# Kernel optimization log

Measured on AMD Instinct MI355X. Metric: run time of the kernel, lower is better.

## Reference

```python
import jax, jax.numpy as jnp
import numpy as np

B, T, ENC, DEC, ATTN = 64, 2048, 512, 512, 256


def setup_inputs() -> dict:
    key = jax.random.key(0)
    k1, k2, k3, k4, k5, k6 = jax.random.split(key, 6)
    enc_out = jax.random.normal(k1, (B, T, ENC), dtype=jnp.float32)
    dec_hidden = jax.random.normal(k2, (B, DEC), dtype=jnp.float32)
    mask = jax.random.randint(k3, (B, T), 0, 2) == 1  # True = masked out
    # learned params (Linear with bias=False); torch Linear weight is [out,in],
    # we store transposed [in,out] for x @ W convention
    s_enc = 1.0 / np.sqrt(ENC)
    s_dec = 1.0 / np.sqrt(DEC)
    s_v = 1.0 / np.sqrt(ATTN)
    W_enc = jax.random.uniform(k4, (ENC, ATTN), jnp.float32, -s_enc, s_enc)
    W_dec = jax.random.uniform(k5, (DEC, ATTN), jnp.float32, -s_dec, s_dec)
    v = jax.random.uniform(k6, (ATTN,), jnp.float32, -s_v, s_v)
    return {"enc_out": enc_out, "dec_hidden": dec_hidden, "mask": mask,
            "W_enc": W_enc, "W_dec": W_dec, "v": v}


def reference(enc_out, dec_hidden, mask, W_enc, W_dec, v):
    # proj_enc: [B,T,A]; proj_dec: [B,1,A]
    proj_enc = jnp.einsum('bte,ea->bta', enc_out, W_enc)
    proj_dec = jnp.einsum('bd,da->ba', dec_hidden, W_dec)[:, None, :]
    # energy: [B,T] -- additive (Bahdanau) score
    energy = jnp.einsum('bta,a->bt', jnp.tanh(proj_enc + proj_dec), v)
    energy = jnp.where(mask, -jnp.inf, energy)
    attn_w = jax.nn.softmax(energy, axis=-1)
    attn_w = jnp.nan_to_num(attn_w, nan=0.0)  # fully-masked rows -> 0
    context = jnp.einsum('bt,bte->be', attn_w, enc_out)
    return context, attn_w
```

## Files before the change

### kernel.cpp

```cpp
#include <hip/hip_runtime.h>
#include <stdint.h>

#define Bx 64
#define Tx 2048
#define ENCx 512
#define ATTx 256

typedef float f4 __attribute__((ext_vector_type(4)));
typedef float f32x4 __attribute__((ext_vector_type(4)));
typedef short bf16x8 __attribute__((ext_vector_type(8)));
typedef __fp16 h2 __attribute__((ext_vector_type(2)));

__device__ __forceinline__ unsigned short f2bf(float f) {
  union { float f; uint32_t u; } c; c.f = f;
  uint32_t u = c.u;
  u += 0x7fffu + ((u >> 16) & 1u);
  return (unsigned short)(u >> 16);
}

__device__ __forceinline__ uint32_t pk_bf(float lo, float hi) {
  uint32_t a = __float_as_uint(lo) + 0x8000u;
  uint32_t b = __float_as_uint(hi) + 0x8000u;
  return __builtin_amdgcn_perm(b, a, 0x07060302u);
}

__device__ __forceinline__ uint32_t pk_f16(float lo, float hi) {
  h2 r = __builtin_amdgcn_cvt_pkrtz(lo, hi);
  union { h2 h; uint32_t u; } c; c.h = r;
  return c.u;
}

__device__ __forceinline__ float ftanh(float x) {
  x = fminf(8.f, fmaxf(-8.f, x));
  float z = __expf(2.f * x);
  return 1.f - __fdividef(2.f, z + 1.f);
}

__global__ void k0_wt(const float* __restrict__ W, unsigned short* __restrict__ WTc) {
  int tid = blockIdx.x * 256 + threadIdx.x;
  int kc = tid >> 13;
  int r = tid & 8191;
  int n = r >> 5;
  int kk = r & 31;
  WTc[tid] = f2bf(W[(kc * 32 + kk) * ATTx + n]);
}

__global__ void k1_pd(const float* __restrict__ dec, const float* __restrict__ Wd,
                      float* __restrict__ pd) {
  __shared__ float ld[512];
  int b = blockIdx.x, a = threadIdx.x;
  ld[a] = dec[b * 512 + a];
  ld[a + 256] = dec[b * 512 + a + 256];
  __syncthreads();
  float s = 0.f;
#pragma unroll 8
  for (int d = 0; d < 512; ++d) s = fmaf(ld[d], Wd[d * ATTx + a], s);
  pd[b * ATTx + a] = s;
}

__global__ __launch_bounds__(128, 1) void k2_fused(
    const float* __restrict__ enc, const unsigned short* __restrict__ WTc,
    const float* __restrict__ pd, const float* __restrict__ v,
    const int* __restrict__ mask, float* __restrict__ energy,
    float* __restrict__ part, float* __restrict__ mloc, float* __restrict__ lloc) {
  __shared__ float pdv[256];
  __shared__ float vvs[256];
  __shared__ unsigned short enc_s[64 * 512];
  __shared__ float e_lds[64];
  __shared__ float wl[64];

  const int tid = threadIdx.x;
  const int wid = tid >> 6;
  const int lane = tid & 63;
  const int q = lane >> 4;
  const int c15 = lane & 15;
  const int m0 = blockIdx.x * 64;
  const int b = m0 >> 11;
  const int chunk = blockIdx.x & 31;

  pdv[tid] = pd[b * ATTx + tid];
  pdv[tid + 128] = pd[b * ATTx + tid + 128];
  vvs[tid] = v[tid];
  vvs[tid + 128] = v[tid + 128];
  __syncthreads();

  const int r0 = wid * 32 + c15;
  const int mrow = m0 + r0;
  const float* a0p = enc + (size_t)mrow * ENCx + q * 8;
  const float* a1p = a0p + 16 * ENCx;
  const unsigned short* wb = WTc + c15 * 32 + q * 8;

  uint4* enc16 = (uint4*)enc_s;
  const int sw = r0 & 7;
  const int w0base = r0 * 64 + q;
  const int w1base = (r0 + 16) * 64 + q;

  f32x4 acc[2][16];
#pragma unroll
  for (int mt = 0; mt < 2; ++mt)
#pragma unroll
    for (int ct = 0; ct < 16; ++ct) { f32x4 z = {0.f,0.f,0.f,0.f}; acc[mt][ct] = z; }

  f4 x0 = *(const f4*)(a0p);
  f4 x1 = *(const f4*)(a0p + 4);
  f4 y0 = *(const f4*)(a1p);
  f4 y1 = *(const f4*)(a1p + 4);

  for (int kc = 0; kc < 16; ++kc) {
    bf16x8 bfr[16];
    const unsigned short* wkc = wb + kc * 8192;
#pragma unroll
    for (int ct = 0; ct < 16; ++ct)
      bfr[ct] = *(const bf16x8*)(wkc + ct * 512);

    const int kn = (kc < 15) ? kc + 1 : 15;
    f4 nx0 = *(const f4*)(a0p + kn * 32);
    f4 nx1 = *(const f4*)(a0p + kn * 32 + 4);
    f4 ny0 = *(const f4*)(a1p + kn * 32);
    f4 ny1 = *(const f4*)(a1p + kn * 32 + 4);

    uint4 hp0, hp1;
    hp0.x = pk_f16(x0.x, x0.y); hp0.y = pk_f16(x0.z, x0.w);
    hp0.z = pk_f16(x1.x, x1.y); hp0.w = pk_f16(x1.z, x1.w);
    hp1.x = pk_f16(y0.x, y0.y); hp1.y = pk_f16(y0.z, y0.w);
    hp1.z = pk_f16(y1.x, y1.y); hp1.w = pk_f16(y1.z, y1.w);
    enc16[(w0base + kc * 4) ^ sw] = hp0;
    enc16[(w1base + kc * 4) ^ sw] = hp1;

    union { uint32_t u[4]; bf16x8 v; } am0, am1;
    am0.u[0] = pk_bf(x0.x, x0.y); am0.u[1] = pk_bf(x0.z, x0.w);
    am0.u[2] = pk_bf(x1.x, x1.y); am0.u[3] = pk_bf(x1.z, x1.w);
    am1.u[0] = pk_bf(y0.x, y0.y); am1.u[1] = pk_bf(y0.z, y0.w);
    am1.u[2] = pk_bf(y1.x, y1.y); am1.u[3] = pk_bf(y1.z, y1.w);

#pragma unroll
    for (int ct = 0; ct < 16; ++ct) {
      acc[0][ct] = __builtin_amdgcn_mfma_f32_16x16x32_bf16(am0.v, bfr[ct], acc[0][ct], 0, 0, 0);
      acc[1][ct] = __builtin_amdgcn_mfma_f32_16x16x32_bf16(am1.v, bfr[ct], acc[1][ct], 0, 0, 0);
    }
    x0 = nx0; x1 = nx1; y0 = ny0; y1 = ny1;
  }

  float ps[2][4];
#pragma unroll
  for (int mt = 0; mt < 2; ++mt)
#pragma unroll
    for (int i = 0; i < 4; ++i) ps[mt][i] = 0.f;
#pragma unroll
  for (int ct = 0; ct < 16; ++ct) {
    float pv = pdv[ct * 16 + c15];
    float vv = vvs[ct * 16 + c15];
#pragma unroll
    for (int mt = 0; mt < 2; ++mt)
#pragma unroll
      for (int i = 0; i < 4; ++i)
        ps[mt][i] += ftanh(acc[mt][ct][i] + pv) * vv;
  }
#pragma unroll
  for (int s = 1; s < 16; s <<= 1)
#pragma unroll
    for (int mt = 0; mt < 2; ++mt)
#pragma unroll
      for (int i = 0; i < 4; ++i)
        ps[mt][i] += __shfl_xor(ps[mt][i], s, 64);
  if (c15 == 0) {
#pragma unroll
    for (int mt = 0; mt < 2; ++mt)
#pragma unroll
      for (int i = 0; i < 4; ++i) {
        int lr = wid * 32 + mt * 16 + q * 4 + i;
        int gm = m0 + lr;
        float ev = mask[gm] ? -1e30f : ps[mt][i];
        energy[gm] = ev;
        e_lds[lr] = ev;
      }
  }
  __syncthreads();

  float ev = e_lds[lane];
  float mx = ev;
#pragma unroll
  for (int s = 1; s < 64; s <<= 1) mx = fmaxf(mx, __shfl_xor(mx, s, 64));
  float w = (ev < -1e29f) ? 0.f : __expf(ev - mx);
  float ls = w;
#pragma unroll
  for (int s = 1; s < 64; s <<= 1) ls += __shfl_xor(ls, s, 64);
  if (wid == 0) wl[lane] = w;
  if (tid == 0) { mloc[b * 32 + chunk] = mx; lloc[b * 32 + chunk] = ls; }
  __syncthreads();

  const uint32_t* encu = (const uint32_t*)enc_s;
  float a0 = 0.f, a1 = 0.f, a2 = 0.f, a3 = 0.f;
#pragma unroll 4
  for (int t = 0; t < 64; ++t) {
    float wv = wl[t];
    int xr = (t & 7) << 2;
    uint32_t p0 = encu[(t * 256 + tid) ^ xr];
    uint32_t p1 = encu[(t * 256 + tid + 128) ^ xr];
    union { uint32_t u; h2 h; } c0, c1;
    c0.u = p0; c1.u = p1;
    a0 = fmaf((float)c0.h.x, wv, a0);
    a1 = fmaf((float)c0.h.y, wv, a1);
    a2 = fmaf((float)c1.h.x, wv, a2);
    a3 = fmaf((float)c1.h.y, wv, a3);
  }
  float* pp = part + (size_t)(chunk * 64 + b) * 512;
  float2 s0; s0.x = a0; s0.y = a1;
  float2 s1; s1.x = a2; s1.y = a3;
  *(float2*)(pp + 2 * tid) = s0;
  *(float2*)(pp + 2 * tid + 256) = s1;
}

__global__ void k3_merge(const float* __restrict__ energy, const float* __restrict__ part,
                         const float* __restrict__ mloc, const float* __restrict__ lloc,
                         float* __restrict__ attn, float* __restrict__ ctx) {
  __shared__ float redm[4];
  __shared__ float redl[4];
  __shared__ float sc[32];
  int b = blockIdx.x, tid = threadIdx.x;
  int lane = tid & 63, wid = tid >> 6;

  float e[8];
#pragma unroll
  for (int i = 0; i < 8; ++i) e[i] = energy[b * Tx + tid + i * 256];
  float m = e[0];
#pragma unroll
  for (int i = 1; i < 8; ++i) m = fmaxf(m, e[i]);
#pragma unroll
  for (int s = 1; s < 64; s <<= 1) m = fmaxf(m, __shfl_xor(m, s, 64));
  if (lane == 0) redm[wid] = m;
  __syncthreads();
  m = fmaxf(fmaxf(redm[0], redm[1]), fmaxf(redm[2], redm[3]));
  bool dead = (m < -1e29f);
  float w[8];
  float l = 0.f;
#pragma unroll
  for (int i = 0; i < 8; ++i) { w[i] = dead ? 0.f : __expf(e[i] - m); l += w[i]; }
#pragma unroll
  for (int s = 1; s < 64; s <<= 1) l += __shfl_xor(l, s, 64);
  if (lane == 0) redl[wid] = l;
  __syncthreads();
  l = redl[0] + redl[1] + redl[2] + redl[3];
  float inv = dead ? 0.f : __fdividef(1.f, l);
#pragma unroll
  for (int i = 0; i < 8; ++i) attn[b * Tx + tid + i * 256] = w[i] * inv;

  if (tid < 64) {
    float mc = (lane < 32) ? mloc[b * 32 + lane] : -3e38f;
    float lc = (lane < 32) ? lloc[b * 32 + lane] : 0.f;
    float mg = mc;
#pragma unroll
    for (int s = 1; s < 64; s <<= 1) mg = fmaxf(mg, __shfl_xor(mg, s, 64));
    float sl = (lane < 32) ? lc * __expf(mc - mg) : 0.f;
    float lg = sl;
#pragma unroll
    for (int s = 1; s < 64; s <<= 1) lg += __shfl_xor(lg, s, 64);
    float ig = (lg > 0.f) ? __fdividef(1.f, lg) : 0.f;
    if (lane < 32) sc[lane] = __expf(mc - mg) * ig;
  }
  __syncthreads();
  float2 a; a.x = 0.f; a.y = 0.f;
  const float* pb = part + (size_t)b * 512 + tid * 2;
#pragma unroll 8
  for (int c = 0; c < 32; ++c) {
    float2 p = *(const float2*)(pb + (size_t)c * 64 * 512);
    float s = sc[c];
    a.x = fmaf(p.x, s, a.x);
    a.y = fmaf(p.y, s, a.y);
  }
  *(float2*)(ctx + b * 512 + tid * 2) = a;
}

extern "C" void kernel_launch(void* const* d_in, const int* in_sizes, int n_in,
                              void* d_out, int out_size, void* d_ws, size_t ws_size,
                              hipStream_t stream) {
  const float* enc   = (const float*)d_in[0];
  const float* dec   = (const float*)d_in[1];
  const int*   mask  = (const int*)d_in[2];
  const float* W_enc = (const float*)d_in[3];
  const float* W_dec = (const float*)d_in[4];
  const float* v     = (const float*)d_in[5];
  float* ctx  = (float*)d_out;
  float* attn = ctx + Bx * ENCx;
  char* ws = (char*)d_ws;
  unsigned short* WTc = (unsigned short*)ws;
  float* pd     = (float*)(ws + 262144);
  float* energy = (float*)(ws + 262144 + 65536);
  float* part   = (float*)(ws + 851968);
  float* mloc   = (float*)(ws + 851968 + 4194304);
  float* lloc   = (float*)(ws + 851968 + 4194304 + 8192);

  k0_wt<<<512, 256, 0, stream>>>(W_enc, WTc);
  k1_pd<<<64, 256, 0, stream>>>(dec, W_dec, pd);
  k2_fused<<<2048, 128, 0, stream>>>(enc, WTc, pd, v, mask, energy, part, mloc, lloc);
  k3_merge<<<64, 256, 0, stream>>>(energy, part, mloc, lloc, attn, ctx);
}
```

Before: 466.1 us.

## Drop LDS fp16 staging of enc; reread enc from global for context, 128-row blocks

The fused kernel no longer keeps a 64KB fp16 copy of the encoder tile in shared memory for the context pass. It rereads the fp32 rows from global memory (likely L2-resident) instead. Blocks grow to 256 threads covering 128 rows, with occupancy target 3 per CU, and the merge kernel now combines 16 chunks instead of 32. This removes the LDS pressure that limited occupancy to one block and removes the fp16 packing work, at the cost of a second global read of enc.

```diff
diff --git a/kernel.cpp b/kernel.cpp
--- a/kernel.cpp
+++ b/kernel.cpp
@@ -9,7 +9,6 @@
 typedef float f4 __attribute__((ext_vector_type(4)));
 typedef float f32x4 __attribute__((ext_vector_type(4)));
 typedef short bf16x8 __attribute__((ext_vector_type(8)));
-typedef __fp16 h2 __attribute__((ext_vector_type(2)));
 
 __device__ __forceinline__ unsigned short f2bf(float f) {
   union { float f; uint32_t u; } c; c.f = f;
@@ -22,12 +21,6 @@
   uint32_t a = __float_as_uint(lo) + 0x8000u;
   uint32_t b = __float_as_uint(hi) + 0x8000u;
   return __builtin_amdgcn_perm(b, a, 0x07060302u);
-}
-
-__device__ __forceinline__ uint32_t pk_f16(float lo, float hi) {
-  h2 r = __builtin_amdgcn_cvt_pkrtz(lo, hi);
-  union { h2 h; uint32_t u; } c; c.h = r;
-  return c.u;
 }
 
 __device__ __forceinline__ float ftanh(float x) {
@@ -58,42 +51,33 @@
   pd[b * ATTx + a] = s;
 }
 
-__global__ __launch_bounds__(128, 1) void k2_fused(
+__global__ __launch_bounds__(256, 3) void k2_fused(
     const float* __restrict__ enc, const unsigned short* __restrict__ WTc,
     const float* __restrict__ pd, const float* __restrict__ v,
     const int* __restrict__ mask, float* __restrict__ energy,
     float* __restrict__ part, float* __restrict__ mloc, float* __restrict__ lloc) {
   __shared__ float pdv[256];
   __shared__ float vvs[256];
-  __shared__ unsigned short enc_s[64 * 512];
-  __shared__ float e_lds[64];
-  __shared__ float wl[64];
+  __shared__ float e_lds[128];
+  __shared__ float wl[128];
 
   const int tid = threadIdx.x;
   const int wid = tid >> 6;
   const int lane = tid & 63;
   const int q = lane >> 4;
   const int c15 = lane & 15;
-  const int m0 = blockIdx.x * 64;
+  const int m0 = blockIdx.x * 128;
   const int b = m0 >> 11;
-  const int chunk = blockIdx.x & 31;
+  const int chunk = blockIdx.x & 15;
 
   pdv[tid] = pd[b * ATTx + tid];
-  pdv[tid + 128] = pd[b * ATTx + tid + 128];
   vvs[tid] = v[tid];
-  vvs[tid + 128] = v[tid + 128];
-  __syncthreads();
-
-  const int r0 = wid * 32 + c15;
-  const int mrow = m0 + r0;
+  __syncthreads();
+
+  const int mrow = m0 + wid * 32 + c15;
   const float* a0p = enc + (size_t)mrow * ENCx + q * 8;
   const float* a1p = a0p + 16 * ENCx;
   const unsigned short* wb = WTc + c15 * 32 + q * 8;
-
-  uint4* enc16 = (uint4*)enc_s;
-  const int sw = r0 & 7;
-  const int w0base = r0 * 64 + q;
-  const int w1base = (r0 + 16) * 64 + q;
 
   f32x4 acc[2][16];
 #pragma unroll
@@ -118,14 +102,6 @@
     f4 nx1 = *(const f4*)(a0p + kn * 32 + 4);
     f4 ny0 = *(const f4*)(a1p + kn * 32);
     f4 ny1 = *(const f4*)(a1p + kn * 32 + 4);
-
-    uint4 hp0, hp1;
-    hp0.x = pk_f16(x0.x, x0.y); hp0.y = pk_f16(x0.z, x0.w);
-    hp0.z = pk_f16(x1.x, x1.y); hp0.w = pk_f16(x1.z, x1.w);
-    hp1.x = pk_f16(y0.x, y0.y); hp1.y = pk_f16(y0.z, y0.w);
-    hp1.z = pk_f16(y1.x, y1.y); hp1.w = pk_f16(y1.z, y1.w);
-    enc16[(w0base + kc * 4) ^ sw] = hp0;
-    enc16[(w1base + kc * 4) ^ sw] = hp1;
 
     union { uint32_t u[4]; bf16x8 v; } am0, am1;
     am0.u[0] = pk_bf(x0.x, x0.y); am0.u[1] = pk_bf(x0.z, x0.w);
@@ -177,38 +153,31 @@
   }
   __syncthreads();
 
-  float ev = e_lds[lane];
-  float mx = ev;
+  float ev0 = e_lds[lane];
+  float ev1 = e_lds[lane + 64];
+  float mx = fmaxf(ev0, ev1);
 #pragma unroll
   for (int s = 1; s < 64; s <<= 1) mx = fmaxf(mx, __shfl_xor(mx, s, 64));
-  float w = (ev < -1e29f) ? 0.f : __expf(ev - mx);
-  float ls = w;
+  float w0 = (ev0 < -1e29f) ? 0.f : __expf(ev0 - mx);
+  float w1 = (ev1 < -1e29f) ? 0.f : __expf(ev1 - mx);
+  float ls = w0 + w1;
 #pragma unroll
   for (int s = 1; s < 64; s <<= 1) ls += __shfl_xor(ls, s, 64);
-  if (wid == 0) wl[lane] = w;
-  if (tid == 0) { mloc[b * 32 + chunk] = mx; lloc[b * 32 + chunk] = ls; }
-  __syncthreads();
-
-  const uint32_t* encu = (const uint32_t*)enc_s;
-  float a0 = 0.f, a1 = 0.f, a2 = 0.f, a3 = 0.f;
+  if (wid == 0) { wl[lane] = w0; wl[lane + 64] = w1; }
+  if (tid == 0) { mloc[b * 16 + chunk] = mx; lloc[b * 16 + chunk] = ls; }
+  __syncthreads();
+
+  const float2* e2 = (const float2*)(enc + ((size_t)b * Tx + chunk * 128) * ENCx);
+  float ax = 0.f, ay = 0.f;
 #pragma unroll 4
-  for (int t = 0; t < 64; ++t) {
+  for (int t = 0; t < 128; ++t) {
     float wv = wl[t];
-    int xr = (t & 7) << 2;
-    uint32_t p0 = encu[(t * 256 + tid) ^ xr];
-    uint32_t p1 = encu[(t * 256 + tid + 128) ^ xr];
-    union { uint32_t u; h2 h; } c0, c1;
-    c0.u = p0; c1.u = p1;
-    a0 = fmaf((float)c0.h.x, wv, a0);
-    a1 = fmaf((float)c0.h.y, wv, a1);
-    a2 = fmaf((float)c1.h.x, wv, a2);
-    a3 = fmaf((float)c1.h.y, wv, a3);
-  }
-  float* pp = part + (size_t)(chunk * 64 + b) * 512;
-  float2 s0; s0.x = a0; s0.y = a1;
-  float2 s1; s1.x = a2; s1.y = a3;
-  *(float2*)(pp + 2 * tid) = s0;
-  *(float2*)(pp + 2 * tid + 256) = s1;
+    float2 p = e2[(size_t)t * 256 + tid];
+    ax = fmaf(p.x, wv, ax);
+    ay = fmaf(p.y, wv, ay);
+  }
+  float2 r; r.x = ax; r.y = ay;
+  *(float2*)(part + ((size_t)chunk * 64 + b) * 512 + tid * 2) = r;
 }
 
 __global__ void k3_merge(const float* __restrict__ energy, const float* __restrict__ part,
@@ -216,7 +185,7 @@
                          float* __restrict__ attn, float* __restrict__ ctx) {
   __shared__ float redm[4];
   __shared__ float redl[4];
-  __shared__ float sc[32];
+  __shared__ float sc[16];
   int b = blockIdx.x, tid = threadIdx.x;
   int lane = tid & 63, wid = tid >> 6;
 
@@ -246,24 +215,24 @@
   for (int i = 0; i < 8; ++i) attn[b * Tx + tid + i * 256] = w[i] * inv;
 
   if (tid < 64) {
-    float mc = (lane < 32) ? mloc[b * 32 + lane] : -3e38f;
-    float lc = (lane < 32) ? lloc[b * 32 + lane] : 0.f;
+    float mc = (lane < 16) ? mloc[b * 16 + lane] : -3e38f;
+    float lc = (lane < 16) ? lloc[b * 16 + lane] : 0.f;
     float mg = mc;
 #pragma unroll
     for (int s = 1; s < 64; s <<= 1) mg = fmaxf(mg, __shfl_xor(mg, s, 64));
-    float sl = (lane < 32) ? lc * __expf(mc - mg) : 0.f;
+    float sl = (lane < 16) ? lc * __expf(mc - mg) : 0.f;
     float lg = sl;
 #pragma unroll
     for (int s = 1; s < 64; s <<= 1) lg += __shfl_xor(lg, s, 64);
     float ig = (lg > 0.f) ? __fdividef(1.f, lg) : 0.f;
-    if (lane < 32) sc[lane] = __expf(mc - mg) * ig;
+    if (lane < 16) sc[lane] = __expf(mc - mg) * ig;
   }
   __syncthreads();
   float2 a; a.x = 0.f; a.y = 0.f;
   const float* pb = part + (size_t)b * 512 + tid * 2;
-#pragma unroll 8
-  for (int c = 0; c < 32; ++c) {
-    float2 p = *(const float2*)(pb + (size_t)c * 64 * 512);
+#pragma unroll 4
+  for (int c = 0; c < 16; ++c) {
+    float2 p = *(const float2*)(pb + (size_t)c * 32768);
     float s = sc[c];
     a.x = fmaf(p.x, s, a.x);
     a.y = fmaf(p.y, s, a.y);
@@ -285,13 +254,13 @@
   char* ws = (char*)d_ws;
   unsigned short* WTc = (unsigned short*)ws;
   float* pd     = (float*)(ws + 262144);
-  float* energy = (float*)(ws + 262144 + 65536);
+  float* energy = (float*)(ws + 327680);
   float* part   = (float*)(ws + 851968);
-  float* mloc   = (float*)(ws + 851968 + 4194304);
-  float* lloc   = (float*)(ws + 851968 + 4194304 + 8192);
+  float* mloc   = (float*)(ws + 851968 + 2097152);
+  float* lloc   = (float*)(ws + 851968 + 2097152 + 4096);
 
   k0_wt<<<512, 256, 0, stream>>>(W_enc, WTc);
   k1_pd<<<64, 256, 0, stream>>>(dec, W_dec, pd);
-  k2_fused<<<2048, 128, 0, stream>>>(enc, WTc, pd, v, mask, energy, part, mloc, lloc);
+  k2_fused<<<1024, 256, 0, stream>>>(enc, WTc, pd, v, mask, energy, part, mloc, lloc);
   k3_merge<<<64, 256, 0, stream>>>(energy, part, mloc, lloc, attn, ctx);
 }
```

Measured after the change: 506.6 us. 1.09x slower.
